# Kernel tuning notes

Hardware: AMD Instinct MI355X
Metric: run time of the kernel (lower is better)

Reference implementation:

```python
import jax, jax.numpy as jnp
import numpy as np

N = 12288          # total points across all clouds in the batch
NUM_CLOUDS = 8     # number of point clouds (batch ids)
D_POS = 3          # 3D coordinates
K = 20             # neighbors per point (includes self, loop=True)


def setup_inputs() -> dict:
    key = jax.random.key(0)
    kx, kb = jax.random.split(key)
    x = jax.random.normal(kx, (N, D_POS), dtype=jnp.float32)
    # sorted batch vector with variable-size groups, as torch_cluster expects
    batch = jnp.sort(jax.random.randint(kb, (N,), 0, NUM_CLOUDS, dtype=jnp.int32))
    return {"x": x, "batch": batch, "k": K}


def reference(x, batch, k):
    # positions = x (d=None -> use all columns), cast to float as in the module
    pos = x.astype(jnp.float32)                       # [N, d]
    sq = jnp.sum(pos * pos, axis=1)                   # [N]
    # squared euclidean pairwise distances: [N, N]
    dist = sq[:, None] + sq[None, :] - 2.0 * (pos @ pos.T)
    # batch-aware masking: neighbors must come from the same cloud
    same_cloud = batch[:, None] == batch[None, :]     # [N, N] bool
    dist = jnp.where(same_cloud, dist, jnp.inf)
    # k smallest distances per row; loop=True so self (dist ~ 0) is included
    _, neighbor_indices = jax.lax.top_k(-dist, k)     # [N, k] int32
    return neighbor_indices
```

## Files before the change

### kernel.cpp

```cpp
#include <hip/hip_runtime.h>
#include <stdint.h>


#define MAXC 28
#define ROWS_PER_BLOCK 4

__device__ __forceinline__ unsigned int map32(float d) {
    unsigned int u = __float_as_uint(d);
    return u ^ (unsigned int)(((int)u >> 31) | 0x80000000);
}

__device__ __forceinline__ unsigned long long map64(double d) {
    unsigned long long u = __double_as_longlong(d);
    return u ^ (unsigned long long)(((long long)u >> 63) |
                                    (long long)0x8000000000000000ull);
}

__device__ __forceinline__ unsigned int umin2(unsigned int a, unsigned int b) {
    return a < b ? a : b;
}
__device__ __forceinline__ unsigned int umax2(unsigned int a, unsigned int b) {
    return a > b ? a : b;
}

__device__ __forceinline__ unsigned int wave_umin_dpp(unsigned int v) {
    int x = (int)v, t;
    t = __builtin_amdgcn_update_dpp(-1, x, 0x111, 0xf, 0xf, false);
    x = (int)umin2((unsigned int)x, (unsigned int)t);
    t = __builtin_amdgcn_update_dpp(-1, x, 0x112, 0xf, 0xf, false);
    x = (int)umin2((unsigned int)x, (unsigned int)t);
    t = __builtin_amdgcn_update_dpp(-1, x, 0x114, 0xf, 0xf, false);
    x = (int)umin2((unsigned int)x, (unsigned int)t);
    t = __builtin_amdgcn_update_dpp(-1, x, 0x118, 0xf, 0xf, false);
    x = (int)umin2((unsigned int)x, (unsigned int)t);
    t = __builtin_amdgcn_update_dpp(-1, x, 0x142, 0xa, 0xf, false);
    x = (int)umin2((unsigned int)x, (unsigned int)t);
    t = __builtin_amdgcn_update_dpp(-1, x, 0x143, 0xc, 0xf, false);
    x = (int)umin2((unsigned int)x, (unsigned int)t);
    return (unsigned int)__builtin_amdgcn_readlane(x, 63);
}

__device__ __forceinline__ int wave_lower_bound(const int* __restrict__ arr,
                                                int n, int key, int lane) {
    int lo = 0, len = n;
    while (len > 64) {
        int seg = (len + 63) >> 6;
        int p = lo + lane * seg;
        bool lt = false;
        if (p < lo + len && p < n) lt = (arr[p] < key);
        int c = (int)__popcll(__ballot(lt));
        if (c == 0) return lo;
        int nlo = lo + (c - 1) * seg + 1;
        int hi = lo + c * seg;
        int wend = lo + len;
        if (hi > wend) hi = wend;
        len = hi + 1 - nlo;
        lo = nlo;
    }
    bool lt = false;
    {
        int p = lo + lane;
        if (lane < len && p < n) lt = (arr[p] < key);
    }
    return lo + (int)__popcll(__ballot(lt));
}

__global__ __launch_bounds__(256) void knn_fused_kernel(
        const float* __restrict__ x,
        const int* __restrict__ batch,
        int k, int n,
        int* __restrict__ out) {
#pragma clang fp contract(off)
    __shared__ int coll[ROWS_PER_BLOCK][64];
    const int wave = threadIdx.x >> 6;
    const int lane = threadIdx.x & 63;
    const int i = blockIdx.x * ROWS_PER_BLOCK + wave;
    if (i >= n) return;

    const int b = batch[i];
    const int s0 = wave_lower_bound(batch, n, b, lane);
    const int e0 = wave_lower_bound(batch, n, b + 1, lane);

    const float xi0 = x[3 * i + 0];
    const float xi1 = x[3 * i + 1];
    const float xi2 = x[3 * i + 2];
    const float sqi = xi0 * xi0 + xi1 * xi1 + xi2 * xi2;

    unsigned int slots[MAXC];
    unsigned int c0 = 0xFFFFFFFFu, c1 = 0xFFFFFFFFu;
    unsigned int c2 = 0xFFFFFFFFu, c3 = 0xFFFFFFFFu;
#pragma unroll
    for (int t = 0; t < MAXC; ++t) {
        const int j = s0 + lane + t * 64;
        unsigned int key = 0xFFFFFFFFu;
        if (j < e0) {
            const float y0 = x[3 * j + 0];
            const float y1 = x[3 * j + 1];
            const float y2 = x[3 * j + 2];
            const float sqj = y0 * y0 + y1 * y1 + y2 * y2;
            float dot = __builtin_fmaf(xi2, y2,
                        __builtin_fmaf(xi1, y1, xi0 * y0));
            float d = (sqi + sqj) - 2.0f * dot;
            key = map32(d);
        }
        slots[t] = key;
        switch (t & 3) {
            case 0: c0 = umin2(c0, key); break;
            case 1: c1 = umin2(c1, key); break;
            case 2: c2 = umin2(c2, key); break;
            default: c3 = umin2(c3, key); break;
        }
    }
    unsigned int localmin = umin2(umin2(c0, c1), umin2(c2, c3));

    unsigned int v = localmin;
#pragma unroll
    for (int kk = 2; kk <= 64; kk <<= 1) {
#pragma unroll
        for (int j = kk >> 1; j > 0; j >>= 1) {
            unsigned int p = (unsigned int)__shfl_xor((int)v, j);
            bool keepMin = (((lane & j) == 0) == ((lane & kk) == 0));
            v = keepMin ? umin2(v, p) : umax2(v, p);
        }
    }
    unsigned int T = (unsigned int)__builtin_amdgcn_readlane((int)v, k - 1);

    int base = 0;
#pragma unroll
    for (int t = 0; t < MAXC; ++t) {
        const int j = s0 + lane + t * 64;
        bool hit = (slots[t] <= T) && (j < e0);
        unsigned long long bal = __ballot(hit);
        int off = base + __builtin_amdgcn_mbcnt_hi(
                             (unsigned int)(bal >> 32),
                             __builtin_amdgcn_mbcnt_lo((unsigned int)bal, 0));
        if (hit && off < 64) coll[wave][off] = j;
        base += (int)__popcll(bal);
    }

    if (base > 64) {
        unsigned int thrp1 = 0;
        for (int r = 0; r < k; ++r) {
            unsigned int m0 = slots[0] - thrp1, m1 = slots[1] - thrp1;
            unsigned int m2 = slots[2] - thrp1, m3 = slots[3] - thrp1;
#pragma unroll
            for (int t = 4; t < MAXC; t += 4) {
                m0 = umin2(m0, slots[t + 0] - thrp1);
                m1 = umin2(m1, slots[t + 1] - thrp1);
                m2 = umin2(m2, slots[t + 2] - thrp1);
                m3 = umin2(m3, slots[t + 3] - thrp1);
            }
            unsigned int lm = umin2(umin2(m0, m1), umin2(m2, m3));
            T = wave_umin_dpp(lm) + thrp1;
            thrp1 = T + 1;
        }
        base = 0;
#pragma unroll
        for (int t = 0; t < MAXC; ++t) {
            const int j = s0 + lane + t * 64;
            bool hit = (slots[t] <= T) && (j < e0);
            unsigned long long bal = __ballot(hit);
            int off = base + __builtin_amdgcn_mbcnt_hi(
                                 (unsigned int)(bal >> 32),
                                 __builtin_amdgcn_mbcnt_lo((unsigned int)bal, 0));
            if (hit && off < 64) coll[wave][off] = j;
            base += (int)__popcll(bal);
        }
    }
    const int cnt = base < 64 ? base : 64;

    const bool valid = (lane < cnt);
    const int idx = valid ? coll[wave][lane] : 0;
    unsigned int v32 = 0xFFFFFFFFu;
    unsigned long long m64 = ~0ull;
    if (valid) {
        const float y0 = x[3 * idx + 0];
        const float y1 = x[3 * idx + 1];
        const float y2 = x[3 * idx + 2];
        const float sqj = y0 * y0 + y1 * y1 + y2 * y2;
        float dot = __builtin_fmaf(xi2, y2,
                    __builtin_fmaf(xi1, y1, xi0 * y0));
        float d = (sqi + sqj) - 2.0f * dot;
        v32 = map32(d);
        double q0 = (double)xi0 * (double)xi0;
        double q1 = (double)xi1 * (double)xi1;
        double q2 = (double)xi2 * (double)xi2;
        double sqdi = (q0 + q1) + q2;
        double w0 = (double)y0 * (double)y0;
        double w1 = (double)y1 * (double)y1;
        double w2 = (double)y2 * (double)y2;
        double sqdj = (w0 + w1) + w2;
        double p0 = (double)xi0 * (double)y0;
        double p1 = (double)xi1 * (double)y1;
        double p2 = (double)xi2 * (double)y2;
        double dot64 = (p0 + p1) + p2;
        double d64 = (sqdi + sqdj) - 2.0 * dot64;
        m64 = map64(d64);
    }

    int pos = 0;
    for (int s = 0; s < cnt; ++s) {
        unsigned int vs = (unsigned int)__shfl((int)v32, s);
        unsigned long long ms = __shfl(m64, s);
        int is_ = __shfl(idx, s);
        bool less = (vs < v32) ||
                    (vs == v32 && (ms < m64 || (ms == m64 && is_ < idx)));
        pos += less ? 1 : 0;
    }

    if (valid && pos < k) out[(long long)i * k + pos] = idx;
}

extern "C" void kernel_launch(void* const* d_in, const int* in_sizes, int n_in,
                              void* d_out, int out_size, void* d_ws, size_t ws_size,
                              hipStream_t stream) {
    const float* x = (const float*)d_in[0];
    const int* batch = (const int*)d_in[1];
    const int n = in_sizes[1];
    const int k = out_size / n;
    int* out = (int*)d_out;

    const int blocks = (n + ROWS_PER_BLOCK - 1) / ROWS_PER_BLOCK;
    knn_fused_kernel<<<blocks, 64 * ROWS_PER_BLOCK, 0, stream>>>(x, batch, k, n, out);
}
```

Measured before the change: 94.10 us.

## Precompute per-cloud bounds and padded float4 point layout before kNN kernel

Adds three small pre-kernels: they find each cloud's start and end in the batch vector, then scatter points into a padded per-cloud float4 array (x, y, z, squared norm) with an index map. The main kernel drops its two per-wave binary searches, the per-element bounds checks and the norm recomputation, and reads one aligned float4 per candidate. Padding entries carry huge sentinel distances so no masking is needed. In exchange it adds three launches, and it hardcodes 8 clouds and at most 1792 points per cloud (MAXC*64), so larger clouds would break.

```diff
diff --git a/kernel.cpp b/kernel.cpp
--- a/kernel.cpp
+++ b/kernel.cpp
@@ -3,6 +3,8 @@
 
 
 #define MAXC 28
+#define PADC 1792
+#define NCLOUDS 8
 #define ROWS_PER_BLOCK 4
 
 __device__ __forceinline__ unsigned int map32(float d) {
@@ -40,34 +42,52 @@
     return (unsigned int)__builtin_amdgcn_readlane(x, 63);
 }
 
-__device__ __forceinline__ int wave_lower_bound(const int* __restrict__ arr,
-                                                int n, int key, int lane) {
-    int lo = 0, len = n;
-    while (len > 64) {
-        int seg = (len + 63) >> 6;
-        int p = lo + lane * seg;
-        bool lt = false;
-        if (p < lo + len && p < n) lt = (arr[p] < key);
-        int c = (int)__popcll(__ballot(lt));
-        if (c == 0) return lo;
-        int nlo = lo + (c - 1) * seg + 1;
-        int hi = lo + c * seg;
-        int wend = lo + len;
-        if (hi > wend) hi = wend;
-        len = hi + 1 - nlo;
-        lo = nlo;
-    }
-    bool lt = false;
-    {
-        int p = lo + lane;
-        if (lane < len && p < n) lt = (arr[p] < key);
-    }
-    return lo + (int)__popcll(__ballot(lt));
+__global__ void init_bounds_kernel(int* __restrict__ starts,
+                                   int* __restrict__ ends, int n) {
+    int c = threadIdx.x;
+    starts[c] = n;
+    ends[c] = 0;
+}
+
+__global__ void bounds_kernel(const int* __restrict__ batch, int n,
+                              int* __restrict__ starts, int* __restrict__ ends) {
+    int j = blockIdx.x * blockDim.x + threadIdx.x;
+    if (j >= n) return;
+    int b = batch[j];
+    if (j == 0 || batch[j - 1] != b) starts[b] = j;
+    if (j == n - 1 || batch[j + 1] != b) ends[b] = j + 1;
+}
+
+__global__ void scatter_kernel(const float* __restrict__ x,
+                               const int* __restrict__ starts,
+                               const int* __restrict__ ends,
+                               float4* __restrict__ pts,
+                               int* __restrict__ idxmap) {
+#pragma clang fp contract(off)
+    int p = blockIdx.x * blockDim.x + threadIdx.x;
+    if (p >= NCLOUDS * PADC) return;
+    int c = p / PADC;
+    int r = p - c * PADC;
+    int s = starts[c];
+    int j = s + r;
+    if (j < ends[c]) {
+        float x0 = x[3 * j + 0];
+        float x1 = x[3 * j + 1];
+        float x2 = x[3 * j + 2];
+        float sq = x0 * x0 + x1 * x1 + x2 * x2;
+        pts[p] = make_float4(x0, x1, x2, sq);
+        idxmap[p] = j;
+    } else {
+        pts[p] = make_float4(1e18f, 1e18f, 1e18f, 3e36f);
+        idxmap[p] = -1;
+    }
 }
 
 __global__ __launch_bounds__(256) void knn_fused_kernel(
-        const float* __restrict__ x,
+        const float4* __restrict__ pts,
+        const int* __restrict__ idxmap,
         const int* __restrict__ batch,
+        const int* __restrict__ starts,
         int k, int n,
         int* __restrict__ out) {
 #pragma clang fp contract(off)
@@ -78,31 +98,22 @@
     if (i >= n) return;
 
     const int b = batch[i];
-    const int s0 = wave_lower_bound(batch, n, b, lane);
-    const int e0 = wave_lower_bound(batch, n, b + 1, lane);
-
-    const float xi0 = x[3 * i + 0];
-    const float xi1 = x[3 * i + 1];
-    const float xi2 = x[3 * i + 2];
-    const float sqi = xi0 * xi0 + xi1 * xi1 + xi2 * xi2;
+    const int cbase = b * PADC;
+    const int ip = cbase + (i - starts[b]);
+    const float4 wi4 = pts[ip];
+    const float xi0 = wi4.x, xi1 = wi4.y, xi2 = wi4.z, sqi = wi4.w;
 
     unsigned int slots[MAXC];
     unsigned int c0 = 0xFFFFFFFFu, c1 = 0xFFFFFFFFu;
     unsigned int c2 = 0xFFFFFFFFu, c3 = 0xFFFFFFFFu;
 #pragma unroll
     for (int t = 0; t < MAXC; ++t) {
-        const int j = s0 + lane + t * 64;
-        unsigned int key = 0xFFFFFFFFu;
-        if (j < e0) {
-            const float y0 = x[3 * j + 0];
-            const float y1 = x[3 * j + 1];
-            const float y2 = x[3 * j + 2];
-            const float sqj = y0 * y0 + y1 * y1 + y2 * y2;
-            float dot = __builtin_fmaf(xi2, y2,
-                        __builtin_fmaf(xi1, y1, xi0 * y0));
-            float d = (sqi + sqj) - 2.0f * dot;
-            key = map32(d);
-        }
+        const int jp = cbase + lane + t * 64;
+        const float4 wj = pts[jp];
+        float dot = __builtin_fmaf(xi2, wj.z,
+                    __builtin_fmaf(xi1, wj.y, xi0 * wj.x));
+        float d = (sqi + wj.w) - 2.0f * dot;
+        unsigned int key = map32(d);
         slots[t] = key;
         switch (t & 3) {
             case 0: c0 = umin2(c0, key); break;
@@ -128,13 +139,12 @@
     int base = 0;
 #pragma unroll
     for (int t = 0; t < MAXC; ++t) {
-        const int j = s0 + lane + t * 64;
-        bool hit = (slots[t] <= T) && (j < e0);
+        bool hit = (slots[t] <= T);
         unsigned long long bal = __ballot(hit);
         int off = base + __builtin_amdgcn_mbcnt_hi(
                              (unsigned int)(bal >> 32),
                              __builtin_amdgcn_mbcnt_lo((unsigned int)bal, 0));
-        if (hit && off < 64) coll[wave][off] = j;
+        if (hit && off < 64) coll[wave][off] = cbase + lane + t * 64;
         base += (int)__popcll(bal);
     }
 
@@ -157,42 +167,40 @@
         base = 0;
 #pragma unroll
         for (int t = 0; t < MAXC; ++t) {
-            const int j = s0 + lane + t * 64;
-            bool hit = (slots[t] <= T) && (j < e0);
+            bool hit = (slots[t] <= T);
             unsigned long long bal = __ballot(hit);
             int off = base + __builtin_amdgcn_mbcnt_hi(
                                  (unsigned int)(bal >> 32),
                                  __builtin_amdgcn_mbcnt_lo((unsigned int)bal, 0));
-            if (hit && off < 64) coll[wave][off] = j;
+            if (hit && off < 64) coll[wave][off] = cbase + lane + t * 64;
             base += (int)__popcll(bal);
         }
     }
     const int cnt = base < 64 ? base : 64;
 
     const bool valid = (lane < cnt);
-    const int idx = valid ? coll[wave][lane] : 0;
+    const int jp = valid ? coll[wave][lane] : cbase;
     unsigned int v32 = 0xFFFFFFFFu;
     unsigned long long m64 = ~0ull;
+    int oidx = 0;
     if (valid) {
-        const float y0 = x[3 * idx + 0];
-        const float y1 = x[3 * idx + 1];
-        const float y2 = x[3 * idx + 2];
-        const float sqj = y0 * y0 + y1 * y1 + y2 * y2;
-        float dot = __builtin_fmaf(xi2, y2,
-                    __builtin_fmaf(xi1, y1, xi0 * y0));
-        float d = (sqi + sqj) - 2.0f * dot;
+        const float4 wj = pts[jp];
+        oidx = idxmap[jp];
+        float dot = __builtin_fmaf(xi2, wj.z,
+                    __builtin_fmaf(xi1, wj.y, xi0 * wj.x));
+        float d = (sqi + wj.w) - 2.0f * dot;
         v32 = map32(d);
         double q0 = (double)xi0 * (double)xi0;
         double q1 = (double)xi1 * (double)xi1;
         double q2 = (double)xi2 * (double)xi2;
         double sqdi = (q0 + q1) + q2;
-        double w0 = (double)y0 * (double)y0;
-        double w1 = (double)y1 * (double)y1;
-        double w2 = (double)y2 * (double)y2;
+        double w0 = (double)wj.x * (double)wj.x;
+        double w1 = (double)wj.y * (double)wj.y;
+        double w2 = (double)wj.z * (double)wj.z;
         double sqdj = (w0 + w1) + w2;
-        double p0 = (double)xi0 * (double)y0;
-        double p1 = (double)xi1 * (double)y1;
-        double p2 = (double)xi2 * (double)y2;
+        double p0 = (double)xi0 * (double)wj.x;
+        double p1 = (double)xi1 * (double)wj.y;
+        double p2 = (double)xi2 * (double)wj.z;
         double dot64 = (p0 + p1) + p2;
         double d64 = (sqdi + sqdj) - 2.0 * dot64;
         m64 = map64(d64);
@@ -202,13 +210,13 @@
     for (int s = 0; s < cnt; ++s) {
         unsigned int vs = (unsigned int)__shfl((int)v32, s);
         unsigned long long ms = __shfl(m64, s);
-        int is_ = __shfl(idx, s);
+        int is_ = __shfl(oidx, s);
         bool less = (vs < v32) ||
-                    (vs == v32 && (ms < m64 || (ms == m64 && is_ < idx)));
+                    (vs == v32 && (ms < m64 || (ms == m64 && is_ < oidx)));
         pos += less ? 1 : 0;
     }
 
-    if (valid && pos < k) out[(long long)i * k + pos] = idx;
+    if (valid && pos < k) out[(long long)i * k + pos] = oidx;
 }
 
 extern "C" void kernel_launch(void* const* d_in, const int* in_sizes, int n_in,
@@ -220,6 +228,15 @@
     const int k = out_size / n;
     int* out = (int*)d_out;
 
+    char* ws = (char*)d_ws;
+    float4* pts = (float4*)ws;            ws += (size_t)NCLOUDS * PADC * sizeof(float4);
+    int* idxmap = (int*)ws;               ws += (size_t)NCLOUDS * PADC * sizeof(int);
+    int* starts = (int*)ws;               ws += 256 * sizeof(int);
+    int* ends = (int*)ws;
+
+    init_bounds_kernel<<<1, 256, 0, stream>>>(starts, ends, n);
+    bounds_kernel<<<(n + 255) / 256, 256, 0, stream>>>(batch, n, starts, ends);
+    scatter_kernel<<<(NCLOUDS * PADC + 255) / 256, 256, 0, stream>>>(x, starts, ends, pts, idxmap);
     const int blocks = (n + ROWS_PER_BLOCK - 1) / ROWS_PER_BLOCK;
-    knn_fused_kernel<<<blocks, 64 * ROWS_PER_BLOCK, 0, stream>>>(x, batch, k, n, out);
-}
+    knn_fused_kernel<<<blocks, 64 * ROWS_PER_BLOCK, 0, stream>>>(pts, idxmap, batch, starts, k, n, out);
+}
```

New measurement: 97.27 us. +3.4%, slower.
